# Kernel optimization log

Measured on AMD Instinct MI355X. Metric: run time of the kernel, lower is better.

## Reference

```python
import jax, jax.numpy as jnp
import numpy as np

N_NODES = 50000
N_EDGES = 600000
DIM = 128
N_HEADS = 3
EDGE_VOCAB = 22754
NEG_SLOPE = 0.2


def setup_inputs() -> dict:
    key = jax.random.key(0)
    ks = jax.random.split(key, 12)
    s = 1.0 / np.sqrt(DIM)
    return {
        "x": jax.random.normal(ks[0], (N_NODES, DIM), dtype=jnp.float32),
        "edge_index": jax.random.randint(ks[1], (2, N_EDGES), 0, N_NODES, dtype=jnp.int64),
        "edge_ids": jax.random.randint(ks[2], (N_EDGES,), 0, EDGE_VOCAB, dtype=jnp.int64),
        "ddi_weight": jax.random.uniform(ks[3], (N_EDGES,), dtype=jnp.float32),
        "W_lin": jax.random.normal(ks[4], (DIM, DIM), dtype=jnp.float32) * s,
        "b_lin": jnp.zeros((DIM,), dtype=jnp.float32),
        "edge_emb": jax.random.normal(ks[5], (EDGE_VOCAB, 1), dtype=jnp.float32) * 0.1,
        "W_heads": jax.random.normal(ks[6], (N_HEADS, DIM, DIM), dtype=jnp.float32) * s,
        "att_src": jax.random.normal(ks[7], (N_HEADS, DIM), dtype=jnp.float32) * s,
        "att_dst": jax.random.normal(ks[8], (N_HEADS, DIM), dtype=jnp.float32) * s,
        "bias_heads": jnp.zeros((N_HEADS, DIM), dtype=jnp.float32),
    }


def _gat_head(x, src, dst, ew, W, a_src, a_dst, bias):
    # x: [N, D] (already passed through shared lin), ew: [E] scalar edge weights
    h = x @ W                                   # [N, D]
    e = jax.nn.leaky_relu(
        (h @ a_src)[src] + (h @ a_dst)[dst], NEG_SLOPE)   # [E]
    # segment softmax over destination nodes
    e_max = jax.ops.segment_max(e, dst, num_segments=N_NODES)   # [N]
    e_exp = jnp.exp(e - e_max[dst])                              # [E]
    denom = jax.ops.segment_sum(e_exp, dst, num_segments=N_NODES)
    alpha = e_exp / jnp.maximum(denom[dst], 1e-16)               # [E]
    msg = (alpha * ew)[:, None] * h[src]                         # [E, D]
    return jax.ops.segment_sum(msg, dst, num_segments=N_NODES) + bias


def reference(x, edge_index, edge_ids, ddi_weight, W_lin, b_lin, edge_emb,
              W_heads, att_src, att_dst, bias_heads):
    x = x @ W_lin + b_lin                         # shared linear projection
    ew = edge_emb[edge_ids, 0] - ddi_weight        # [E]
    src, dst = edge_index[0], edge_index[1]
    out = jnp.zeros_like(x)
    for hix in range(N_HEADS):                     # small fixed head count
        out = out + _gat_head(x, src, dst, ew, W_heads[hix],
                              att_src[hix], att_dst[hix], bias_heads[hix])
    return out / N_HEADS
```

## Files before the change

### kernel.cpp

```cpp
#include <hip/hip_runtime.h>
#include <math.h>

#define NN 50000
#define NE 600000
#define D 128
#define NH 3
#define CAP 64
#define EDGE_BLOCKS ((NE + 255) / 256)
#define MFMA_BLOCKS ((NN + 63) / 64)

typedef short bf16x8 __attribute__((ext_vector_type(8)));
typedef float f32x4 __attribute__((ext_vector_type(4)));

__device__ __forceinline__ unsigned short f2b(float f) {
  unsigned int u = __float_as_uint(f);
  u += 0x7FFF + ((u >> 16) & 1);
  return (unsigned short)(u >> 16);
}
__device__ __forceinline__ float blo(unsigned int u) {
  return __uint_as_float(u << 16);
}
__device__ __forceinline__ float bhi(unsigned int u) {
  return __uint_as_float(u & 0xffff0000u);
}
__device__ __forceinline__ float b2f(unsigned short us) {
  return __uint_as_float((unsigned int)us << 16);
}
__device__ __forceinline__ unsigned short f2h(float f) {
  _Float16 t = (_Float16)f;
  return *(unsigned short*)&t;
}
__device__ __forceinline__ float h2f(unsigned short us) {
  _Float16 t = *(_Float16*)&us;
  return (float)t;
}

__global__ __launch_bounds__(256) void pack_scatter2(const float* __restrict__ W_lin,
                                                     const float* __restrict__ W_heads,
                                                     const float* __restrict__ att_src,
                                                     const float* __restrict__ att_dst,
                                                     const float* __restrict__ b_lin,
                                                     const float* __restrict__ bias_heads,
                                                     const int* __restrict__ ei,
                                                     const int* __restrict__ eid,
                                                     const float* __restrict__ ddi,
                                                     const float* __restrict__ emb,
                                                     uint4* __restrict__ Bpack,
                                                     uint4* __restrict__ Wpack3,
                                                     float* __restrict__ sbuf,
                                                     float* __restrict__ bcomb2,
                                                     int* __restrict__ counts,
                                                     unsigned int* __restrict__ slots8) {
  const int bx = blockIdx.x;
  const int tid = threadIdx.x;
  if (bx < EDGE_BLOCKS) {
    int e = bx * 256 + tid;
    if (e < NE) {
      int src = ei[e], dst = ei[NE + e];
      int idx = atomicAdd(&counts[dst], 1);
      idx = idx < CAP ? idx : CAP - 1;
      float ew = emb[eid[e]] - ddi[e];
      slots8[dst * CAP + idx] = (unsigned int)src | ((unsigned int)f2b(ew) << 16);
    }
    return;
  }
  const int pb = bx - EDGE_BLOCKS;
  if (pb < 8) {
    int r = pb * 256 + tid;
    int nt = r >> 8, s = (r >> 6) & 3, q = (r >> 4) & 3, n0 = r & 15;
    int kbase = s * 32 + q * 8;
    int n = nt * 16 + n0;
    unsigned int w[4];
    #pragma unroll
    for (int p = 0; p < 4; ++p) {
      unsigned short lo = f2b(W_lin[(kbase + 2 * p) * D + n]);
      unsigned short hi = f2b(W_lin[(kbase + 2 * p + 1) * D + n]);
      w[p] = (unsigned int)lo | ((unsigned int)hi << 16);
    }
    Bpack[r] = make_uint4(w[0], w[1], w[2], w[3]);
  } else if (pb < 32) {
    int u = (pb - 8) * 256 + tid;
    int h = u >> 11, r = u & 2047;
    int nt = r >> 8, s = (r >> 6) & 3, q = (r >> 4) & 3, n0 = r & 15;
    int kbase = s * 32 + q * 8;
    int n = nt * 16 + n0;
    const float* W = W_heads + (size_t)h * D * D;
    unsigned int w[4];
    #pragma unroll
    for (int p = 0; p < 4; ++p) {
      unsigned short lo = f2b(W[(kbase + 2 * p) * D + n]);
      unsigned short hi = f2b(W[(kbase + 2 * p + 1) * D + n]);
      w[p] = (unsigned int)lo | ((unsigned int)hi << 16);
    }
    Wpack3[h * 2048 + r] = make_uint4(w[0], w[1], w[2], w[3]);
  } else if (pb < 35) {
    const int h = pb - 32;
    __shared__ float wha_s[128], wha_d[128], scs[128], scd[128];
    {
      int m = tid & 127;
      const float* W = W_heads + (size_t)h * D * D + m * D;
      const float* a = (tid < 128) ? (att_src + h * D) : (att_dst + h * D);
      float acc = 0.f;
      for (int n = 0; n < D; ++n) acc += W[n] * a[n];
      if (tid < 128) wha_s[m] = acc; else wha_d[m] = acc;
    }
    __syncthreads();
    {
      int k = tid & 127;
      const float* wl = W_lin + k * D;
      const float* wha = (tid < 128) ? wha_s : wha_d;
      float acc = 0.f;
      for (int m = 0; m < D; ++m) acc += wl[m] * wha[m];
      if (tid < 128) scs[k] = acc; else scd[k] = acc;
    }
    __syncthreads();
    if (tid < 2) {
      const float* wha = tid ? wha_d : wha_s;
      float a = 0.f;
      for (int k = 0; k < D; ++k) a += b_lin[k] * wha[k];
      sbuf[h * 2 + tid] = a;
    }
    {
      int s = (tid >> 6) & 3, q = (tid >> 4) & 3, n0 = tid & 15;
      int kbase = s * 32 + q * 8;
      bool mine = (n0 < 6) && ((n0 >> 1) == h);
      bool zero = (h == 0) && (n0 >= 6);
      if (mine || zero) {
        float vals[8];
        #pragma unroll
        for (int j = 0; j < 8; ++j)
          vals[j] = zero ? 0.f : ((n0 & 1) ? scd[kbase + j] : scs[kbase + j]);
        unsigned int w[4];
        #pragma unroll
        for (int p = 0; p < 4; ++p)
          w[p] = (unsigned int)f2b(vals[2 * p]) | ((unsigned int)f2b(vals[2 * p + 1]) << 16);
        Bpack[2048 + tid] = make_uint4(w[0], w[1], w[2], w[3]);
      }
    }
  } else {
    if (tid < D)
      bcomb2[tid] = (bias_heads[tid] + bias_heads[D + tid] + bias_heads[2 * D + tid]) * (1.f / 3.f);
  }
}

__global__ __launch_bounds__(256) void mfma_x(const float* __restrict__ x,
                                              const uint4* __restrict__ Bpack,
                                              const float* __restrict__ b_lin,
                                              const float* __restrict__ sbuf,
                                              unsigned short* __restrict__ xb,
                                              float* __restrict__ s_src4,
                                              float* __restrict__ s_dst4) {
  const int row0 = blockIdx.x * 64;
  const int tid = threadIdx.x;
  __shared__ __align__(16) unsigned short As[64][136];
  #pragma unroll
  for (int it = 0; it < 8; ++it) {
    int idx = tid + it * 256;
    int m = idx >> 5, k4 = idx & 31;
    int row = row0 + m;
    float4 v = make_float4(0.f, 0.f, 0.f, 0.f);
    if (row < NN) v = ((const float4*)(x + (size_t)row * D))[k4];
    uint2 pk;
    pk.x = (unsigned int)f2b(v.x) | ((unsigned int)f2b(v.y) << 16);
    pk.y = (unsigned int)f2b(v.z) | ((unsigned int)f2b(v.w) << 16);
    *((uint2*)&As[m][k4 * 4]) = pk;
  }
  __syncthreads();
  const int wv = tid >> 6;
  const int lane = tid & 63;
  const int n0 = lane & 15, q = lane >> 4;
  const int boff = q * 16 + n0;
  const bf16x8* Bp = (const bf16x8*)Bpack;

  bf16x8 a4[4];
  #pragma unroll
  for (int s = 0; s < 4; ++s)
    a4[s] = *(const bf16x8*)&As[wv * 16 + n0][s * 32 + q * 8];

  f32x4 acc[9];
  #pragma unroll
  for (int nt = 0; nt < 9; ++nt) acc[nt] = (f32x4){0.f, 0.f, 0.f, 0.f};

  #pragma unroll
  for (int s = 0; s < 4; ++s) {
    #pragma unroll
    for (int nt = 0; nt < 9; ++nt) {
      bf16x8 b = Bp[(nt * 4 + s) * 64 + boff];
      acc[nt] = __builtin_amdgcn_mfma_f32_16x16x32_bf16(a4[s], b, acc[nt], 0, 0, 0);
    }
  }
  __syncthreads();
  #pragma unroll
  for (int nt = 0; nt < 8; ++nt) {
    int col = nt * 16 + n0;
    float bv = b_lin[col];
    #pragma unroll
    for (int r = 0; r < 4; ++r)
      As[wv * 16 + q * 4 + r][col] = f2b(acc[nt][r] + bv);
  }
  if (n0 < 6) {
    float sb = sbuf[n0];
    float* Sout = (n0 & 1) ? s_dst4 : s_src4;
    #pragma unroll
    for (int r = 0; r < 4; ++r) {
      int row = row0 + wv * 16 + q * 4 + r;
      if (row < NN) Sout[row * 4 + (n0 >> 1)] = acc[8][r] + sb;
    }
  }
  __syncthreads();
  #pragma unroll
  for (int i = 0; i < 4; ++i) {
    int idx = tid + i * 256;
    int row = idx >> 4, c16 = idx & 15;
    int grow = row0 + row;
    if (grow < NN)
      *((uint4*)&xb[(size_t)grow * D + c16 * 8]) = *((const uint4*)&As[row][c16 * 8]);
  }
}

__global__ __launch_bounds__(64) void gather12(const int* __restrict__ counts,
                                               const unsigned int* __restrict__ slots8,
                                               const float4* __restrict__ s_src4,
                                               const float4* __restrict__ s_dst4,
                                               const unsigned short* __restrict__ xb,
                                               unsigned short* __restrict__ accb) {
  const int dst = blockIdx.x;
  const int lane = threadIdx.x;
  const int hf = lane >> 5;
  const int c = (lane & 31) * 4;
  int cnt = counts[dst];
  cnt = cnt < CAP ? cnt : CAP;
  const int beg = dst * CAP;
  const int end = beg + cnt;
  float4 sd = s_dst4[dst];
  float a0[4] = {0.f, 0.f, 0.f, 0.f};
  float a1[4] = {0.f, 0.f, 0.f, 0.f};
  float a2[4] = {0.f, 0.f, 0.f, 0.f};
  float d0 = 0.f, d1 = 0.f, d2 = 0.f;
  int s = beg + hf;
  for (; s + 2 < end; s += 4) {
    unsigned int seA = slots8[s];
    unsigned int seB = slots8[s + 2];
    int srcA = seA & 0xffffu, srcB = seB & 0xffffu;
    float ewA = bhi(seA), ewB = bhi(seB);
    float4 ssA = s_src4[srcA];
    float4 ssB = s_src4[srcB];
    uint2 ua = *(const uint2*)&xb[(size_t)srcA * D + c];
    uint2 ub = *(const uint2*)&xb[(size_t)srcB * D + c];
    float vA0 = ssA.x + sd.x, vA1 = ssA.y + sd.y, vA2 = ssA.z + sd.z;
    float vB0 = ssB.x + sd.x, vB1 = ssB.y + sd.y, vB2 = ssB.z + sd.z;
    vA0 = vA0 > 0.f ? vA0 : 0.2f * vA0;
    vA1 = vA1 > 0.f ? vA1 : 0.2f * vA1;
    vA2 = vA2 > 0.f ? vA2 : 0.2f * vA2;
    vB0 = vB0 > 0.f ? vB0 : 0.2f * vB0;
    vB1 = vB1 > 0.f ? vB1 : 0.2f * vB1;
    vB2 = vB2 > 0.f ? vB2 : 0.2f * vB2;
    float pA0 = __expf(vA0), pA1 = __expf(vA1), pA2 = __expf(vA2);
    float pB0 = __expf(vB0), pB1 = __expf(vB1), pB2 = __expf(vB2);
    float wa0 = pA0 * ewA, wa1 = pA1 * ewA, wa2 = pA2 * ewA;
    float wb0 = pB0 * ewB, wb1 = pB1 * ewB, wb2 = pB2 * ewB;
    float xA[4] = {blo(ua.x), bhi(ua.x), blo(ua.y), bhi(ua.y)};
    float xB[4] = {blo(ub.x), bhi(ub.x), blo(ub.y), bhi(ub.y)};
    #pragma unroll
    for (int j = 0; j < 4; ++j) {
      a0[j] += wa0 * xA[j] + wb0 * xB[j];
      a1[j] += wa1 * xA[j] + wb1 * xB[j];
      a2[j] += wa2 * xA[j] + wb2 * xB[j];
    }
    d0 += pA0 + pB0;
    d1 += pA1 + pB1;
    d2 += pA2 + pB2;
  }
  if (s < end) {
    unsigned int seA = slots8[s];
    int srcA = seA & 0xffffu;
    float ewA = bhi(seA);
    float4 ssA = s_src4[srcA];
    uint2 ua = *(const uint2*)&xb[(size_t)srcA * D + c];
    float vA0 = ssA.x + sd.x, vA1 = ssA.y + sd.y, vA2 = ssA.z + sd.z;
    vA0 = vA0 > 0.f ? vA0 : 0.2f * vA0;
    vA1 = vA1 > 0.f ? vA1 : 0.2f * vA1;
    vA2 = vA2 > 0.f ? vA2 : 0.2f * vA2;
    float pA0 = __expf(vA0), pA1 = __expf(vA1), pA2 = __expf(vA2);
    float w0 = pA0 * ewA, w1 = pA1 * ewA, w2 = pA2 * ewA;
    float xA[4] = {blo(ua.x), bhi(ua.x), blo(ua.y), bhi(ua.y)};
    #pragma unroll
    for (int j = 0; j < 4; ++j) {
      a0[j] += w0 * xA[j];
      a1[j] += w1 * xA[j];
      a2[j] += w2 * xA[j];
    }
    d0 += pA0; d1 += pA1; d2 += pA2;
  }
  #pragma unroll
  for (int j = 0; j < 4; ++j) {
    a0[j] += __shfl_xor(a0[j], 32, 64);
    a1[j] += __shfl_xor(a1[j], 32, 64);
    a2[j] += __shfl_xor(a2[j], 32, 64);
  }
  d0 += __shfl_xor(d0, 32, 64);
  d1 += __shfl_xor(d1, 32, 64);
  d2 += __shfl_xor(d2, 32, 64);
  if (hf == 0) {
    float r0 = 1.f / (3.f * fmaxf(d0, 1e-16f));
    float r1 = 1.f / (3.f * fmaxf(d1, 1e-16f));
    float r2 = 1.f / (3.f * fmaxf(d2, 1e-16f));
    unsigned short* base = accb + (size_t)dst * (NH * D);
    uint2 o;
    o.x = (unsigned int)f2h(a0[0] * r0) | ((unsigned int)f2h(a0[1] * r0) << 16);
    o.y = (unsigned int)f2h(a0[2] * r0) | ((unsigned int)f2h(a0[3] * r0) << 16);
    *(uint2*)&base[c] = o;
    o.x = (unsigned int)f2h(a1[0] * r1) | ((unsigned int)f2h(a1[1] * r1) << 16);
    o.y = (unsigned int)f2h(a1[2] * r1) | ((unsigned int)f2h(a1[3] * r1) << 16);
    *(uint2*)&base[D + c] = o;
    o.x = (unsigned int)f2h(a2[0] * r2) | ((unsigned int)f2h(a2[1] * r2) << 16);
    o.y = (unsigned int)f2h(a2[2] * r2) | ((unsigned int)f2h(a2[3] * r2) << 16);
    *(uint2*)&base[2 * D + c] = o;
  }
}

__global__ __launch_bounds__(256) void final_gemm(const unsigned short* __restrict__ accb,
                                                  const uint4* __restrict__ Wpack3,
                                                  const float* __restrict__ bcomb2,
                                                  float* __restrict__ out) {
  const int row0 = blockIdx.x * 64;
  const int tid = threadIdx.x;
  __shared__ __align__(16) unsigned short Ah[64][136];
  __shared__ __align__(16) unsigned short Al[64][136];
  const int wv = tid >> 6;
  const int lane = tid & 63;
  const int n0 = lane & 15, q = lane >> 4;
  const int boff = q * 16 + n0;

  f32x4 o[8];
  #pragma unroll
  for (int nt = 0; nt < 8; ++nt) o[nt] = (f32x4){0.f, 0.f, 0.f, 0.f};

  for (int chunk = 0; chunk < NH; ++chunk) {
    if (chunk) __syncthreads();
    #pragma unroll
    for (int it = 0; it < 4; ++it) {
      int idx = tid + it * 256;
      int m = idx >> 4, k8 = idx & 15;
      int row = row0 + m;
      uint4 u = make_uint4(0, 0, 0, 0);
      if (row < NN)
        u = *(const uint4*)&accb[(size_t)row * (NH * D) + chunk * D + k8 * 8];
      const unsigned int* pu = (const unsigned int*)&u;
      unsigned int hw[2], lw[2];
      #pragma unroll
      for (int p = 0; p < 2; ++p) {
        unsigned short hh[4], ll[4];
        #pragma unroll
        for (int e = 0; e < 2; ++e) {
          unsigned int word = pu[2 * p + e];
          float f0 = h2f((unsigned short)(word & 0xffffu));
          float f1 = h2f((unsigned short)(word >> 16));
          unsigned short h0 = f2b(f0), h1 = f2b(f1);
          hh[2 * e] = h0; hh[2 * e + 1] = h1;
          ll[2 * e] = f2b(f0 - b2f(h0));
          ll[2 * e + 1] = f2b(f1 - b2f(h1));
        }
        hw[p] = (unsigned int)hh[0] | ((unsigned int)hh[1] << 16);
        lw[p] = (unsigned int)ll[0] | ((unsigned int)ll[1] << 16);
        hw[p] |= 0; lw[p] |= 0;
        if (true) {
          ((unsigned int*)&Ah[m][k8 * 8])[2 * p]     = (unsigned int)hh[0] | ((unsigned int)hh[1] << 16);
          ((unsigned int*)&Ah[m][k8 * 8])[2 * p + 1] = (unsigned int)hh[2] | ((unsigned int)hh[3] << 16);
          ((unsigned int*)&Al[m][k8 * 8])[2 * p]     = (unsigned int)ll[0] | ((unsigned int)ll[1] << 16);
          ((unsigned int*)&Al[m][k8 * 8])[2 * p + 1] = (unsigned int)ll[2] | ((unsigned int)ll[3] << 16);
        }
      }
    }
    __syncthreads();
    bf16x8 ah[4], al[4];
    #pragma unroll
    for (int s = 0; s < 4; ++s) {
      ah[s] = *(const bf16x8*)&Ah[wv * 16 + n0][s * 32 + q * 8];
      al[s] = *(const bf16x8*)&Al[wv * 16 + n0][s * 32 + q * 8];
    }
    const bf16x8* Bp = (const bf16x8*)(Wpack3 + chunk * 2048);
    #pragma unroll
    for (int s = 0; s < 4; ++s) {
      #pragma unroll
      for (int nt = 0; nt < 8; ++nt) {
        bf16x8 b = Bp[(nt * 4 + s) * 64 + boff];
        o[nt] = __builtin_amdgcn_mfma_f32_16x16x32_bf16(ah[s], b, o[nt], 0, 0, 0);
        o[nt] = __builtin_amdgcn_mfma_f32_16x16x32_bf16(al[s], b, o[nt], 0, 0, 0);
      }
    }
  }
  #pragma unroll
  for (int nt = 0; nt < 8; ++nt) {
    int col = nt * 16 + n0;
    float bv = bcomb2[col];
    #pragma unroll
    for (int r = 0; r < 4; ++r) {
      int row = row0 + wv * 16 + q * 4 + r;
      if (row < NN) out[(size_t)row * D + col] = o[nt][r] + bv;
    }
  }
}

extern "C" void kernel_launch(void* const* d_in, const int* in_sizes, int n_in,
                              void* d_out, int out_size, void* d_ws, size_t ws_size,
                              hipStream_t stream) {
  const float* x          = (const float*)d_in[0];
  const int*   ei         = (const int*)d_in[1];
  const int*   eid        = (const int*)d_in[2];
  const float* ddi        = (const float*)d_in[3];
  const float* W_lin      = (const float*)d_in[4];
  const float* b_lin      = (const float*)d_in[5];
  const float* emb        = (const float*)d_in[6];
  const float* W_heads    = (const float*)d_in[7];
  const float* att_src    = (const float*)d_in[8];
  const float* att_dst    = (const float*)d_in[9];
  const float* bias_heads = (const float*)d_in[10];
  float* out = (float*)d_out;

  uint4*  Bpack  = (uint4*)d_ws;
  uint4*  Wpack3 = Bpack + 2304;
  unsigned short* xb = (unsigned short*)(Wpack3 + NH * 2048);
  unsigned int* slots8 = (unsigned int*)(xb + (size_t)NN * D);
  unsigned short* accb = (unsigned short*)(slots8 + (size_t)NN * CAP);
  float*  sbuf   = (float*)(accb + (size_t)NN * NH * D);
  float*  bcomb2 = sbuf + 8;
  float*  s_src4 = bcomb2 + 128;
  float*  s_dst4 = s_src4 + (size_t)NN * 4;
  int*    counts = (int*)(s_dst4 + (size_t)NN * 4);

  hipMemsetAsync(counts, 0, (size_t)NN * sizeof(int), stream);
  pack_scatter2<<<EDGE_BLOCKS + 36, 256, 0, stream>>>(
      W_lin, W_heads, att_src, att_dst, b_lin, bias_heads, ei, eid, ddi, emb,
      Bpack, Wpack3, sbuf, bcomb2, counts, slots8);
  mfma_x<<<MFMA_BLOCKS, 256, 0, stream>>>(x, Bpack, b_lin, sbuf, xb,
                                          s_src4, s_dst4);
  gather12<<<NN, 64, 0, stream>>>(counts, slots8, (const float4*)s_src4,
                                  (const float4*)s_dst4, xb, accb);
  final_gemm<<<MFMA_BLOCKS, 256, 0, stream>>>(accb, Wpack3, bcomb2, out);
}
```

Before: 234.3 us.

## Fuse gather aggregation with final head GEMM using fp16 MFMA via LDS

Merges the per-destination gather kernel and the final GEMM into one kernel. Each 512-thread block aggregates 64 destination rows into an LDS fp16 tile, then multiplies that tile by the head weights. This removes the global accb round trip and one launch. The head weights are now packed as fp16 and a single f16 MFMA replaces the bf16 hi/lo split pair, halving MFMA work but lowering precision. The costs are reduced parallelism (782 blocks instead of 50000) and about 50KB of LDS per block, which limits occupancy.

```diff
diff --git a/kernel.cpp b/kernel.cpp
--- a/kernel.cpp
+++ b/kernel.cpp
@@ -10,6 +10,7 @@
 #define MFMA_BLOCKS ((NN + 63) / 64)
 
 typedef short bf16x8 __attribute__((ext_vector_type(8)));
+typedef _Float16 f16x8 __attribute__((ext_vector_type(8)));
 typedef float f32x4 __attribute__((ext_vector_type(4)));
 
 __device__ __forceinline__ unsigned short f2b(float f) {
@@ -23,16 +24,9 @@
 __device__ __forceinline__ float bhi(unsigned int u) {
   return __uint_as_float(u & 0xffff0000u);
 }
-__device__ __forceinline__ float b2f(unsigned short us) {
-  return __uint_as_float((unsigned int)us << 16);
-}
 __device__ __forceinline__ unsigned short f2h(float f) {
   _Float16 t = (_Float16)f;
   return *(unsigned short*)&t;
-}
-__device__ __forceinline__ float h2f(unsigned short us) {
-  _Float16 t = *(_Float16*)&us;
-  return (float)t;
 }
 
 __global__ __launch_bounds__(256) void pack_scatter2(const float* __restrict__ W_lin,
@@ -88,8 +82,8 @@
     unsigned int w[4];
     #pragma unroll
     for (int p = 0; p < 4; ++p) {
-      unsigned short lo = f2b(W[(kbase + 2 * p) * D + n]);
-      unsigned short hi = f2b(W[(kbase + 2 * p + 1) * D + n]);
+      unsigned short lo = f2h(W[(kbase + 2 * p) * D + n]);
+      unsigned short hi = f2h(W[(kbase + 2 * p + 1) * D + n]);
       w[p] = (unsigned int)lo | ((unsigned int)hi << 16);
     }
     Wpack3[h * 2048 + r] = make_uint4(w[0], w[1], w[2], w[3]);
@@ -218,186 +212,151 @@
   }
 }
 
-__global__ __launch_bounds__(64) void gather12(const int* __restrict__ counts,
-                                               const unsigned int* __restrict__ slots8,
-                                               const float4* __restrict__ s_src4,
-                                               const float4* __restrict__ s_dst4,
-                                               const unsigned short* __restrict__ xb,
-                                               unsigned short* __restrict__ accb) {
-  const int dst = blockIdx.x;
-  const int lane = threadIdx.x;
+__global__ __launch_bounds__(512) void gfin(const int* __restrict__ counts,
+                                            const unsigned int* __restrict__ slots8,
+                                            const float4* __restrict__ s_src4,
+                                            const float4* __restrict__ s_dst4,
+                                            const unsigned short* __restrict__ xb,
+                                            const uint4* __restrict__ Wpack3,
+                                            const float* __restrict__ bcomb2,
+                                            float* __restrict__ out) {
+  const int row0 = blockIdx.x * 64;
+  const int tid = threadIdx.x;
+  const int wv = tid >> 6;
+  const int lane = tid & 63;
+  __shared__ __align__(16) _Float16 Acc[64][392];
+
   const int hf = lane >> 5;
   const int c = (lane & 31) * 4;
-  int cnt = counts[dst];
-  cnt = cnt < CAP ? cnt : CAP;
-  const int beg = dst * CAP;
-  const int end = beg + cnt;
-  float4 sd = s_dst4[dst];
-  float a0[4] = {0.f, 0.f, 0.f, 0.f};
-  float a1[4] = {0.f, 0.f, 0.f, 0.f};
-  float a2[4] = {0.f, 0.f, 0.f, 0.f};
-  float d0 = 0.f, d1 = 0.f, d2 = 0.f;
-  int s = beg + hf;
-  for (; s + 2 < end; s += 4) {
-    unsigned int seA = slots8[s];
-    unsigned int seB = slots8[s + 2];
-    int srcA = seA & 0xffffu, srcB = seB & 0xffffu;
-    float ewA = bhi(seA), ewB = bhi(seB);
-    float4 ssA = s_src4[srcA];
-    float4 ssB = s_src4[srcB];
-    uint2 ua = *(const uint2*)&xb[(size_t)srcA * D + c];
-    uint2 ub = *(const uint2*)&xb[(size_t)srcB * D + c];
-    float vA0 = ssA.x + sd.x, vA1 = ssA.y + sd.y, vA2 = ssA.z + sd.z;
-    float vB0 = ssB.x + sd.x, vB1 = ssB.y + sd.y, vB2 = ssB.z + sd.z;
-    vA0 = vA0 > 0.f ? vA0 : 0.2f * vA0;
-    vA1 = vA1 > 0.f ? vA1 : 0.2f * vA1;
-    vA2 = vA2 > 0.f ? vA2 : 0.2f * vA2;
-    vB0 = vB0 > 0.f ? vB0 : 0.2f * vB0;
-    vB1 = vB1 > 0.f ? vB1 : 0.2f * vB1;
-    vB2 = vB2 > 0.f ? vB2 : 0.2f * vB2;
-    float pA0 = __expf(vA0), pA1 = __expf(vA1), pA2 = __expf(vA2);
-    float pB0 = __expf(vB0), pB1 = __expf(vB1), pB2 = __expf(vB2);
-    float wa0 = pA0 * ewA, wa1 = pA1 * ewA, wa2 = pA2 * ewA;
-    float wb0 = pB0 * ewB, wb1 = pB1 * ewB, wb2 = pB2 * ewB;
-    float xA[4] = {blo(ua.x), bhi(ua.x), blo(ua.y), bhi(ua.y)};
-    float xB[4] = {blo(ub.x), bhi(ub.x), blo(ub.y), bhi(ub.y)};
-    #pragma unroll
-    for (int j = 0; j < 4; ++j) {
-      a0[j] += wa0 * xA[j] + wb0 * xB[j];
-      a1[j] += wa1 * xA[j] + wb1 * xB[j];
-      a2[j] += wa2 * xA[j] + wb2 * xB[j];
-    }
-    d0 += pA0 + pB0;
-    d1 += pA1 + pB1;
-    d2 += pA2 + pB2;
-  }
-  if (s < end) {
-    unsigned int seA = slots8[s];
-    int srcA = seA & 0xffffu;
-    float ewA = bhi(seA);
-    float4 ssA = s_src4[srcA];
-    uint2 ua = *(const uint2*)&xb[(size_t)srcA * D + c];
-    float vA0 = ssA.x + sd.x, vA1 = ssA.y + sd.y, vA2 = ssA.z + sd.z;
-    vA0 = vA0 > 0.f ? vA0 : 0.2f * vA0;
-    vA1 = vA1 > 0.f ? vA1 : 0.2f * vA1;
-    vA2 = vA2 > 0.f ? vA2 : 0.2f * vA2;
-    float pA0 = __expf(vA0), pA1 = __expf(vA1), pA2 = __expf(vA2);
-    float w0 = pA0 * ewA, w1 = pA1 * ewA, w2 = pA2 * ewA;
-    float xA[4] = {blo(ua.x), bhi(ua.x), blo(ua.y), bhi(ua.y)};
-    #pragma unroll
-    for (int j = 0; j < 4; ++j) {
-      a0[j] += w0 * xA[j];
-      a1[j] += w1 * xA[j];
-      a2[j] += w2 * xA[j];
-    }
-    d0 += pA0; d1 += pA1; d2 += pA2;
-  }
-  #pragma unroll
-  for (int j = 0; j < 4; ++j) {
-    a0[j] += __shfl_xor(a0[j], 32, 64);
-    a1[j] += __shfl_xor(a1[j], 32, 64);
-    a2[j] += __shfl_xor(a2[j], 32, 64);
-  }
-  d0 += __shfl_xor(d0, 32, 64);
-  d1 += __shfl_xor(d1, 32, 64);
-  d2 += __shfl_xor(d2, 32, 64);
-  if (hf == 0) {
-    float r0 = 1.f / (3.f * fmaxf(d0, 1e-16f));
-    float r1 = 1.f / (3.f * fmaxf(d1, 1e-16f));
-    float r2 = 1.f / (3.f * fmaxf(d2, 1e-16f));
-    unsigned short* base = accb + (size_t)dst * (NH * D);
-    uint2 o;
-    o.x = (unsigned int)f2h(a0[0] * r0) | ((unsigned int)f2h(a0[1] * r0) << 16);
-    o.y = (unsigned int)f2h(a0[2] * r0) | ((unsigned int)f2h(a0[3] * r0) << 16);
-    *(uint2*)&base[c] = o;
-    o.x = (unsigned int)f2h(a1[0] * r1) | ((unsigned int)f2h(a1[1] * r1) << 16);
-    o.y = (unsigned int)f2h(a1[2] * r1) | ((unsigned int)f2h(a1[3] * r1) << 16);
-    *(uint2*)&base[D + c] = o;
-    o.x = (unsigned int)f2h(a2[0] * r2) | ((unsigned int)f2h(a2[1] * r2) << 16);
-    o.y = (unsigned int)f2h(a2[2] * r2) | ((unsigned int)f2h(a2[3] * r2) << 16);
-    *(uint2*)&base[2 * D + c] = o;
-  }
-}
-
-__global__ __launch_bounds__(256) void final_gemm(const unsigned short* __restrict__ accb,
-                                                  const uint4* __restrict__ Wpack3,
-                                                  const float* __restrict__ bcomb2,
-                                                  float* __restrict__ out) {
-  const int row0 = blockIdx.x * 64;
-  const int tid = threadIdx.x;
-  __shared__ __align__(16) unsigned short Ah[64][136];
-  __shared__ __align__(16) unsigned short Al[64][136];
-  const int wv = tid >> 6;
-  const int lane = tid & 63;
+  for (int i = 0; i < 8; ++i) {
+    const int m = wv * 8 + i;
+    const int dst = row0 + m;
+    if (dst < NN) {
+      int cnt = counts[dst];
+      cnt = cnt < CAP ? cnt : CAP;
+      const int beg = dst * CAP;
+      const int end = beg + cnt;
+      float4 sd = s_dst4[dst];
+      float a0[4] = {0.f, 0.f, 0.f, 0.f};
+      float a1[4] = {0.f, 0.f, 0.f, 0.f};
+      float a2[4] = {0.f, 0.f, 0.f, 0.f};
+      float d0 = 0.f, d1 = 0.f, d2 = 0.f;
+      int s = beg + hf;
+      for (; s + 2 < end; s += 4) {
+        unsigned int seA = slots8[s];
+        unsigned int seB = slots8[s + 2];
+        int srcA = seA & 0xffffu, srcB = seB & 0xffffu;
+        float ewA = bhi(seA), ewB = bhi(seB);
+        float4 ssA = s_src4[srcA];
+        float4 ssB = s_src4[srcB];
+        uint2 ua = *(const uint2*)&xb[(size_t)srcA * D + c];
+        uint2 ub = *(const uint2*)&xb[(size_t)srcB * D + c];
+        float vA0 = ssA.x + sd.x, vA1 = ssA.y + sd.y, vA2 = ssA.z + sd.z;
+        float vB0 = ssB.x + sd.x, vB1 = ssB.y + sd.y, vB2 = ssB.z + sd.z;
+        vA0 = vA0 > 0.f ? vA0 : 0.2f * vA0;
+        vA1 = vA1 > 0.f ? vA1 : 0.2f * vA1;
+        vA2 = vA2 > 0.f ? vA2 : 0.2f * vA2;
+        vB0 = vB0 > 0.f ? vB0 : 0.2f * vB0;
+        vB1 = vB1 > 0.f ? vB1 : 0.2f * vB1;
+        vB2 = vB2 > 0.f ? vB2 : 0.2f * vB2;
+        float pA0 = __expf(vA0), pA1 = __expf(vA1), pA2 = __expf(vA2);
+        float pB0 = __expf(vB0), pB1 = __expf(vB1), pB2 = __expf(vB2);
+        float wa0 = pA0 * ewA, wa1 = pA1 * ewA, wa2 = pA2 * ewA;
+        float wb0 = pB0 * ewB, wb1 = pB1 * ewB, wb2 = pB2 * ewB;
+        float xA[4] = {blo(ua.x), bhi(ua.x), blo(ua.y), bhi(ua.y)};
+        float xB[4] = {blo(ub.x), bhi(ub.x), blo(ub.y), bhi(ub.y)};
+        #pragma unroll
+        for (int j = 0; j < 4; ++j) {
+          a0[j] += wa0 * xA[j] + wb0 * xB[j];
+          a1[j] += wa1 * xA[j] + wb1 * xB[j];
+          a2[j] += wa2 * xA[j] + wb2 * xB[j];
+        }
+        d0 += pA0 + pB0;
+        d1 += pA1 + pB1;
+        d2 += pA2 + pB2;
+      }
+      if (s < end) {
+        unsigned int seA = slots8[s];
+        int srcA = seA & 0xffffu;
+        float ewA = bhi(seA);
+        float4 ssA = s_src4[srcA];
+        uint2 ua = *(const uint2*)&xb[(size_t)srcA * D + c];
+        float vA0 = ssA.x + sd.x, vA1 = ssA.y + sd.y, vA2 = ssA.z + sd.z;
+        vA0 = vA0 > 0.f ? vA0 : 0.2f * vA0;
+        vA1 = vA1 > 0.f ? vA1 : 0.2f * vA1;
+        vA2 = vA2 > 0.f ? vA2 : 0.2f * vA2;
+        float pA0 = __expf(vA0), pA1 = __expf(vA1), pA2 = __expf(vA2);
+        float w0 = pA0 * ewA, w1 = pA1 * ewA, w2 = pA2 * ewA;
+        float xA[4] = {blo(ua.x), bhi(ua.x), blo(ua.y), bhi(ua.y)};
+        #pragma unroll
+        for (int j = 0; j < 4; ++j) {
+          a0[j] += w0 * xA[j];
+          a1[j] += w1 * xA[j];
+          a2[j] += w2 * xA[j];
+        }
+        d0 += pA0; d1 += pA1; d2 += pA2;
+      }
+      #pragma unroll
+      for (int j = 0; j < 4; ++j) {
+        a0[j] += __shfl_xor(a0[j], 32, 64);
+        a1[j] += __shfl_xor(a1[j], 32, 64);
+        a2[j] += __shfl_xor(a2[j], 32, 64);
+      }
+      d0 += __shfl_xor(d0, 32, 64);
+      d1 += __shfl_xor(d1, 32, 64);
+      d2 += __shfl_xor(d2, 32, 64);
+      if (hf == 0) {
+        float r0 = 1.f / (3.f * fmaxf(d0, 1e-16f));
+        float r1 = 1.f / (3.f * fmaxf(d1, 1e-16f));
+        float r2 = 1.f / (3.f * fmaxf(d2, 1e-16f));
+        uint2 o;
+        o.x = (unsigned int)f2h(a0[0] * r0) | ((unsigned int)f2h(a0[1] * r0) << 16);
+        o.y = (unsigned int)f2h(a0[2] * r0) | ((unsigned int)f2h(a0[3] * r0) << 16);
+        *(uint2*)&Acc[m][c] = o;
+        o.x = (unsigned int)f2h(a1[0] * r1) | ((unsigned int)f2h(a1[1] * r1) << 16);
+        o.y = (unsigned int)f2h(a1[2] * r1) | ((unsigned int)f2h(a1[3] * r1) << 16);
+        *(uint2*)&Acc[m][D + c] = o;
+        o.x = (unsigned int)f2h(a2[0] * r2) | ((unsigned int)f2h(a2[1] * r2) << 16);
+        o.y = (unsigned int)f2h(a2[2] * r2) | ((unsigned int)f2h(a2[3] * r2) << 16);
+        *(uint2*)&Acc[m][2 * D + c] = o;
+      }
+    }
+  }
+  __syncthreads();
+
   const int n0 = lane & 15, q = lane >> 4;
+  const int rw = wv & 3;
+  const int cb = wv >> 2;
   const int boff = q * 16 + n0;
-
-  f32x4 o[8];
-  #pragma unroll
-  for (int nt = 0; nt < 8; ++nt) o[nt] = (f32x4){0.f, 0.f, 0.f, 0.f};
-
-  for (int chunk = 0; chunk < NH; ++chunk) {
-    if (chunk) __syncthreads();
-    #pragma unroll
-    for (int it = 0; it < 4; ++it) {
-      int idx = tid + it * 256;
-      int m = idx >> 4, k8 = idx & 15;
-      int row = row0 + m;
-      uint4 u = make_uint4(0, 0, 0, 0);
-      if (row < NN)
-        u = *(const uint4*)&accb[(size_t)row * (NH * D) + chunk * D + k8 * 8];
-      const unsigned int* pu = (const unsigned int*)&u;
-      unsigned int hw[2], lw[2];
-      #pragma unroll
-      for (int p = 0; p < 2; ++p) {
-        unsigned short hh[4], ll[4];
-        #pragma unroll
-        for (int e = 0; e < 2; ++e) {
-          unsigned int word = pu[2 * p + e];
-          float f0 = h2f((unsigned short)(word & 0xffffu));
-          float f1 = h2f((unsigned short)(word >> 16));
-          unsigned short h0 = f2b(f0), h1 = f2b(f1);
-          hh[2 * e] = h0; hh[2 * e + 1] = h1;
-          ll[2 * e] = f2b(f0 - b2f(h0));
-          ll[2 * e + 1] = f2b(f1 - b2f(h1));
-        }
-        hw[p] = (unsigned int)hh[0] | ((unsigned int)hh[1] << 16);
-        lw[p] = (unsigned int)ll[0] | ((unsigned int)ll[1] << 16);
-        hw[p] |= 0; lw[p] |= 0;
-        if (true) {
-          ((unsigned int*)&Ah[m][k8 * 8])[2 * p]     = (unsigned int)hh[0] | ((unsigned int)hh[1] << 16);
-          ((unsigned int*)&Ah[m][k8 * 8])[2 * p + 1] = (unsigned int)hh[2] | ((unsigned int)hh[3] << 16);
-          ((unsigned int*)&Al[m][k8 * 8])[2 * p]     = (unsigned int)ll[0] | ((unsigned int)ll[1] << 16);
-          ((unsigned int*)&Al[m][k8 * 8])[2 * p + 1] = (unsigned int)ll[2] | ((unsigned int)ll[3] << 16);
-        }
-      }
-    }
-    __syncthreads();
-    bf16x8 ah[4], al[4];
-    #pragma unroll
-    for (int s = 0; s < 4; ++s) {
-      ah[s] = *(const bf16x8*)&Ah[wv * 16 + n0][s * 32 + q * 8];
-      al[s] = *(const bf16x8*)&Al[wv * 16 + n0][s * 32 + q * 8];
-    }
-    const bf16x8* Bp = (const bf16x8*)(Wpack3 + chunk * 2048);
+  f32x4 o4[4];
+  #pragma unroll
+  for (int nt = 0; nt < 4; ++nt) o4[nt] = (f32x4){0.f, 0.f, 0.f, 0.f};
+
+  #pragma unroll
+  for (int ck = 0; ck < NH; ++ck) {
+    f16x8 af[4];
+    #pragma unroll
+    for (int s = 0; s < 4; ++s)
+      af[s] = *(const f16x8*)&Acc[rw * 16 + n0][ck * D + s * 32 + q * 8];
+    const f16x8* Bp = (const f16x8*)(Wpack3 + ck * 2048);
     #pragma unroll
     for (int s = 0; s < 4; ++s) {
       #pragma unroll
-      for (int nt = 0; nt < 8; ++nt) {
-        bf16x8 b = Bp[(nt * 4 + s) * 64 + boff];
-        o[nt] = __builtin_amdgcn_mfma_f32_16x16x32_bf16(ah[s], b, o[nt], 0, 0, 0);
-        o[nt] = __builtin_amdgcn_mfma_f32_16x16x32_bf16(al[s], b, o[nt], 0, 0, 0);
-      }
-    }
-  }
-  #pragma unroll
-  for (int nt = 0; nt < 8; ++nt) {
-    int col = nt * 16 + n0;
+      for (int nt = 0; nt < 4; ++nt) {
+        int NT = cb * 4 + nt;
+        f16x8 b = Bp[(NT * 4 + s) * 64 + boff];
+        o4[nt] = __builtin_amdgcn_mfma_f32_16x16x32_f16(af[s], b, o4[nt], 0, 0, 0);
+      }
+    }
+  }
+  #pragma unroll
+  for (int nt = 0; nt < 4; ++nt) {
+    int col = cb * 64 + nt * 16 + n0;
     float bv = bcomb2[col];
     #pragma unroll
     for (int r = 0; r < 4; ++r) {
-      int row = row0 + wv * 16 + q * 4 + r;
-      if (row < NN) out[(size_t)row * D + col] = o[nt][r] + bv;
+      int row = row0 + rw * 16 + q * 4 + r;
+      if (row < NN) out[(size_t)row * D + col] = o4[nt][r] + bv;
     }
   }
 }
@@ -422,8 +381,7 @@
   uint4*  Wpack3 = Bpack + 2304;
   unsigned short* xb = (unsigned short*)(Wpack3 + NH * 2048);
   unsigned int* slots8 = (unsigned int*)(xb + (size_t)NN * D);
-  unsigned short* accb = (unsigned short*)(slots8 + (size_t)NN * CAP);
-  float*  sbuf   = (float*)(accb + (size_t)NN * NH * D);
+  float*  sbuf   = (float*)(slots8 + (size_t)NN * CAP);
   float*  bcomb2 = sbuf + 8;
   float*  s_src4 = bcomb2 + 128;
   float*  s_dst4 = s_src4 + (size_t)NN * 4;
@@ -435,7 +393,7 @@
       Bpack, Wpack3, sbuf, bcomb2, counts, slots8);
   mfma_x<<<MFMA_BLOCKS, 256, 0, stream>>>(x, Bpack, b_lin, sbuf, xb,
                                           s_src4, s_dst4);
-  gather12<<<NN, 64, 0, stream>>>(counts, slots8, (const float4*)s_src4,
-                                  (const float4*)s_dst4, xb, accb);
-  final_gemm<<<MFMA_BLOCKS, 256, 0, stream>>>(accb, Wpack3, bcomb2, out);
-}
+  gfin<<<MFMA_BLOCKS, 512, 0, stream>>>(counts, slots8, (const float4*)s_src4,
+                                        (const float4*)s_dst4, xb, Wpack3,
+                                        bcomb2, out);
+}
```

Result: slower. 242.3 us (+3.4%).
